# Optimization experiments

Measured on AMD Instinct MI355X. Metric: run time of the kernel, lower is better.

The kernel has to match this reference:

```python
import jax, jax.numpy as jnp
from jax import lax
from jax.experimental.ode import odeint
import numpy as np

INPUT_DIM, HIDDEN_DIM, LATENT_DIM, OUTPUT_DIM = 6, 64, 16, 1
RTOL, ATOL = 1e-3, 1e-4
NOISE_STD = 0.0  # model_noise=0 -> deterministic drift, faithful to relu(W z + b) + 0
B, T = 2048, 512


def _init(key, shape, fan_in):
    bound = 1.0 / np.sqrt(fan_in)
    return jax.random.uniform(key, shape, jnp.float32, -bound, bound)


def setup_inputs() -> dict:
    key = jax.random.key(0)
    ks = jax.random.split(key, 18)
    inp = {
        "x": jax.random.normal(ks[0], (B, T, INPUT_DIM), jnp.float32),
        # encoder GRU (input 6 -> hidden 64), torch layout: W_ih [3H, D], W_hh [3H, H]
        "enc_Wih": _init(ks[1], (3 * HIDDEN_DIM, INPUT_DIM), HIDDEN_DIM),
        "enc_Whh": _init(ks[2], (3 * HIDDEN_DIM, HIDDEN_DIM), HIDDEN_DIM),
        "enc_bih": _init(ks[3], (3 * HIDDEN_DIM,), HIDDEN_DIM),
        "enc_bhh": _init(ks[4], (3 * HIDDEN_DIM,), HIDDEN_DIM),
        "fc_mu_W": _init(ks[5], (LATENT_DIM, HIDDEN_DIM), HIDDEN_DIM),
        "fc_mu_b": _init(ks[6], (LATENT_DIM,), HIDDEN_DIM),
        "fc_lv_W": _init(ks[7], (LATENT_DIM, HIDDEN_DIM), HIDDEN_DIM),
        "fc_lv_b": _init(ks[8], (LATENT_DIM,), HIDDEN_DIM),
        # latent SDE drift linear 16 -> 16
        "ode_W": _init(ks[9], (LATENT_DIM, LATENT_DIM), LATENT_DIM),
        "ode_b": _init(ks[10], (LATENT_DIM,), LATENT_DIM),
        # decoder fc 16 -> 64, then GRU (input 64 -> hidden 1)
        "dec_fc_W": _init(ks[11], (HIDDEN_DIM, LATENT_DIM), LATENT_DIM),
        "dec_fc_b": _init(ks[12], (HIDDEN_DIM,), LATENT_DIM),
        "dec_Wih": _init(ks[13], (3 * OUTPUT_DIM, HIDDEN_DIM), OUTPUT_DIM),
        "dec_Whh": _init(ks[14], (3 * OUTPUT_DIM, OUTPUT_DIM), OUTPUT_DIM),
        "dec_bih": _init(ks[15], (3 * OUTPUT_DIM,), OUTPUT_DIM),
        "dec_bhh": _init(ks[16], (3 * OUTPUT_DIM,), OUTPUT_DIM),
    }
    return inp


def _gru_cell(h, x_gates, Whh, bhh):
    # x_gates: precomputed x @ Wih.T + bih, shape [B, 3H]; h: [B, H]
    h_gates = h @ Whh.T + bhh
    xr, xz, xn = jnp.split(x_gates, 3, axis=-1)
    hr, hz, hn = jnp.split(h_gates, 3, axis=-1)
    r = jax.nn.sigmoid(xr + hr)
    zg = jax.nn.sigmoid(xz + hz)
    n = jnp.tanh(xn + r * hn)
    return (1.0 - zg) * n + zg * h


def _forward(x, enc_Wih, enc_Whh, enc_bih, enc_bhh, fc_mu_W, fc_mu_b,
             fc_lv_W, fc_lv_b, ode_W, ode_b, dec_fc_W, dec_fc_b,
             dec_Wih, dec_Whh, dec_bih, dec_bhh):
    Bsz, Tlen, _ = x.shape
    # ---- encoder GRU, keep only last hidden state ----
    xg = jnp.einsum('btd,gd->btg', x, enc_Wih) + enc_bih  # [B,T,3H]
    h0 = jnp.zeros((Bsz, HIDDEN_DIM), x.dtype)
    def enc_step(h, xt):
        return _gru_cell(h, xt, enc_Whh, enc_bhh), None
    hT, _ = lax.scan(enc_step, h0, jnp.swapaxes(xg, 0, 1))
    mu = hT @ fc_mu_W.T + fc_mu_b          # [B,16]
    log_var = hT @ fc_lv_W.T + fc_lv_b     # [B,16]
    # deterministic reparam exactly as source: z = mu + sqrt(exp(log_var))
    z0 = mu + jnp.exp(0.5 * log_var)
    # ---- dopri5 adaptive integration of dz/dt = relu(W z + b) on t in [0,1] ----
    def drift(z, t):
        return jax.nn.relu(z @ ode_W.T + ode_b)
    ts = jnp.linspace(0.0, 1.0, 10)
    zs = odeint(drift, z0, ts, rtol=RTOL, atol=ATOL)
    z = zs[-1]                              # [B,16]
    # ---- decoder: relu(fc1), repeat over time, GRU(64->1) ----
    zd = jax.nn.relu(z @ dec_fc_W.T + dec_fc_b)            # [B,64]
    xg_dec = zd @ dec_Wih.T + dec_bih                       # same every step, [B,3]
    hd0 = jnp.zeros((Bsz, OUTPUT_DIM), x.dtype)
    def dec_step(h, _):
        h = _gru_cell(h, xg_dec, dec_Whh, dec_bhh)
        return h, h
    _, outs = lax.scan(dec_step, hd0, None, length=Tlen)    # [T,B,1]
    x_recon = jnp.swapaxes(outs, 0, 1)                      # [B,T,1]
    return x_recon, mu, log_var


def reference(x, enc_Wih, enc_Whh, enc_bih, enc_bhh, fc_mu_W, fc_mu_b,
              fc_lv_W, fc_lv_b, ode_W, ode_b, dec_fc_W, dec_fc_b,
              dec_Wih, dec_Whh, dec_bih, dec_bhh):
    return _forward(x, enc_Wih, enc_Whh, enc_bih, enc_bhh, fc_mu_W, fc_mu_b,
                    fc_lv_W, fc_lv_b, ode_W, ode_b, dec_fc_W, dec_fc_b,
                    dec_Wih, dec_Whh, dec_bih, dec_bhh)
```

## Files before the change

### kernel.cpp

```cpp
#include <hip/hip_runtime.h>
#include <math.h>

#define B_TOTAL 2048
#define T_LEN   512
#define IN_D    6
#define HID     64
#define LAT     16
#define ROWS    4
#define THREADS 256
#define ASTRIDE 104

typedef __attribute__((ext_vector_type(8))) short bfrag;
typedef __attribute__((ext_vector_type(4))) float ffrag;

#if __has_builtin(__builtin_amdgcn_exp2f)
#define EXP2F(x) __builtin_amdgcn_exp2f(x)
#else
#define EXP2F(x) exp2f(x)
#endif
#if __has_builtin(__builtin_amdgcn_rcpf)
#define RCPF(x) __builtin_amdgcn_rcpf(x)
#else
#define RCPF(x) (1.0f / (x))
#endif
#define MFMA16(A, B, C) __builtin_amdgcn_mfma_f32_16x16x32_bf16((A), (B), (C), 0, 0, 0)

__device__ __forceinline__ float fast_sigmoid(float x){
    return RCPF(1.0f + EXP2F(-1.44269504088896340736f * x));
}
__device__ __forceinline__ float fast_tanh(float x){
    return 1.0f - 2.0f * RCPF(EXP2F(2.88539008177792681472f * x) + 1.0f);
}
__device__ __forceinline__ unsigned short f2bf_rne(float f){
    unsigned u = __float_as_uint(f);
    return (unsigned short)((u + 0x7fffu + ((u >> 16) & 1u)) >> 16);
}

extern "C" __global__ void
__attribute__((amdgpu_flat_work_group_size(THREADS, THREADS), amdgpu_waves_per_eu(2, 2)))
glsde_kernel(const float* __restrict__ x,
             const float* __restrict__ eWih, const float* __restrict__ eWhh,
             const float* __restrict__ ebih, const float* __restrict__ ebhh,
             const float* __restrict__ muW,  const float* __restrict__ mub,
             const float* __restrict__ lvW,  const float* __restrict__ lvb,
             const float* __restrict__ oW,   const float* __restrict__ ob,
             const float* __restrict__ dfW,  const float* __restrict__ dfb,
             const float* __restrict__ dWih, const float* __restrict__ dWhh,
             const float* __restrict__ dbih, const float* __restrict__ dbhh,
             float* __restrict__ out)
{
    __shared__ __align__(16) unsigned short xstage[T_LEN][ROWS][8];
    __shared__ __align__(16) unsigned short Abuf[2][16][ASTRIDE];
    __shared__ float hfp[ROWS][HID];
    __shared__ float zsh[ROWS][LAT];
    __shared__ float zdsh[ROWS][HID];
    __shared__ float xgdsh[ROWS][3];

    const int tid  = threadIdx.x;
    const int wave = tid >> 6;
    const int lane = tid & 63;
    const int nloc = lane & 15;
    const int quad = lane >> 4;
    const int mA   = lane & 15;
    const int j    = wave * 16 + nloc;
    const int b0   = blockIdx.x * ROWS;

    const float S1 = 1.44269504088896340736f;
    const float S2 = 2.0f * S1;

    bfrag Br[3], Bz[3], Bnh[2], Bnx;
    {
        const float* wr  = eWhh + (size_t)(      j) * HID;
        const float* wz  = eWhh + (size_t)( 64 + j) * HID;
        const float* wn  = eWhh + (size_t)(128 + j) * HID;
        #pragma unroll
        for (int kt = 0; kt < 2; ++kt){
            const int o = kt * 32 + quad * 8;
            #pragma unroll
            for (int e = 0; e < 8; ++e){
                Br[kt][e]  = (short)f2bf_rne(wr[o+e] * S1);
                Bz[kt][e]  = (short)f2bf_rne(wz[o+e] * S1);
                Bnh[kt][e] = (short)f2bf_rne(wn[o+e] * S2);
            }
        }
        const float* ir  = eWih + (size_t)(      j) * IN_D;
        const float* iz  = eWih + (size_t)( 64 + j) * IN_D;
        const float* inn = eWih + (size_t)(128 + j) * IN_D;
        #pragma unroll
        for (int e = 0; e < 8; ++e){
            bool v = (quad == 0 && e < IN_D);
            Br[2][e] = v ? (short)f2bf_rne(ir[e]  * S1) : (short)0;
            Bz[2][e] = v ? (short)f2bf_rne(iz[e]  * S1) : (short)0;
            Bnx[e]   = v ? (short)f2bf_rne(inn[e] * S2) : (short)0;
        }
    }
    const float bias_r = (ebih[j]      + ebhh[j])      * S1;
    const float bias_z = (ebih[64 + j] + ebhh[64 + j]) * S1;
    const float bihn2  = ebih[128 + j] * S2;
    const float bhhn2  = ebhh[128 + j] * S2;

    {
        unsigned* ap = (unsigned*)Abuf;
        for (int i = tid; i < (int)(sizeof(Abuf) / 4); i += THREADS) ap[i] = 0u;
    }

    for (int idx = tid; idx < T_LEN * ROWS; idx += THREADS){
        const int tt = idx & (T_LEN - 1);
        const int bb = idx >> 9;
        const float* xr = x + (size_t)(b0 + bb) * T_LEN * IN_D + (size_t)tt * IN_D;
        const float2* p2 = (const float2*)xr;
        float2 v0 = p2[0], v1 = p2[1], v2 = p2[2];
        bfrag f;
        f[0] = (short)f2bf_rne(v0.x); f[1] = (short)f2bf_rne(v0.y);
        f[2] = (short)f2bf_rne(v1.x); f[3] = (short)f2bf_rne(v1.y);
        f[4] = (short)f2bf_rne(v2.x); f[5] = (short)f2bf_rne(v2.y);
        f[6] = 0; f[7] = 0;
        *(bfrag*)&xstage[tt][bb][0] = f;
    }
    __syncthreads();

    float hreg = 0.f;

    const unsigned short* xsp = &xstage[0][mA >> 2][0];

    bfrag Ax = *(const bfrag*)(xsp);

#define GRU_STEP(bufR, bufW, T)                                                   \
    do {                                                                          \
        const unsigned short* ah_ = &bufR[mA][0];                                 \
        bfrag Ah0 = *(const bfrag*)(ah_ + 0  + quad * 8);                         \
        bfrag Ah1 = *(const bfrag*)(ah_ + 32 + quad * 8);                         \
        int tn_ = (T) + 1; if (tn_ >= T_LEN) tn_ = T_LEN - 1;                     \
        bfrag AxN = *(const bfrag*)(xsp + (size_t)tn_ * (ROWS * 8));              \
        ffrag aR  = {bias_r, bias_r, bias_r, bias_r};                             \
        ffrag aZ  = {bias_z, bias_z, bias_z, bias_z};                             \
        ffrag aNX = {bihn2,  bihn2,  bihn2,  bihn2 };                             \
        ffrag aNH = {bhhn2,  bhhn2,  bhhn2,  bhhn2 };                             \
                      \
        aR  = MFMA16(Ax,  Br[2],  aR );                                           \
        aZ  = MFMA16(Ax,  Bz[2],  aZ );                                           \
        aNX = MFMA16(Ax,  Bnx,    aNX);                                           \
        aR  = MFMA16(Ah0, Br[0],  aR );                                           \
        aZ  = MFMA16(Ah0, Bz[0],  aZ );                                           \
        aNH = MFMA16(Ah0, Bnh[0], aNH);                                           \
        aR  = MFMA16(Ah1, Br[1],  aR );                                           \
        aZ  = MFMA16(Ah1, Bz[1],  aZ );                                           \
        aNH = MFMA16(Ah1, Bnh[1], aNH);                                           \
        float rg = RCPF(1.0f + EXP2F(-aR[0]));                                    \
        float zg = RCPF(1.0f + EXP2F(-aZ[0]));                                    \
        float yy = aNX[0] + rg * aNH[0];                                          \
        float ng = 1.0f - 2.0f * RCPF(EXP2F(yy) + 1.0f);                          \
        float hn = (1.0f - zg) * ng + zg * hreg;                                  \
        hreg = hn;                                                                \
        bufW[quad * 4][j] = f2bf_rne(hn);                                         \
        Ax = AxN;                                                                 \
        __syncthreads();                                                          \
    } while (0)

    for (int t = 0; t < T_LEN; t += 2){
        GRU_STEP(Abuf[0], Abuf[1], t);
        GRU_STEP(Abuf[1], Abuf[0], t + 1);
    }
#undef GRU_STEP

    hfp[quad][j] = hreg;
    __syncthreads();

    const int zrow = tid >> 4, zi = tid & 15;
    float z0v = 0.0f;
    if (tid < ROWS * LAT){
        float am = mub[zi], al = lvb[zi];
        const float4* pm = (const float4*)(muW + (size_t)zi * HID);
        const float4* pq = (const float4*)(lvW + (size_t)zi * HID);
        const float4* ph = (const float4*)(&hfp[zrow][0]);
        #pragma unroll
        for (int q = 0; q < 16; ++q){
            float4 wm = pm[q], wl = pq[q], hv = ph[q];
            am += wm.x*hv.x + wm.y*hv.y + wm.z*hv.z + wm.w*hv.w;
            al += wl.x*hv.x + wl.y*hv.y + wl.z*hv.z + wl.w*hv.w;
        }
        const size_t muBase = (size_t)B_TOTAL * T_LEN;
        out[muBase + (size_t)(b0 + zrow) * LAT + zi] = am;
        out[muBase + (size_t)B_TOTAL * LAT + (size_t)(b0 + zrow) * LAT + zi] = al;
        z0v = am + __expf(0.5f * al);
    }

    if (tid < ROWS * LAT){
        float ows[16];
        {
            const float4* pw = (const float4*)(oW + (size_t)zi * LAT);
            #pragma unroll
            for (int q = 0; q < 4; ++q){
                float4 w = pw[q];
                ows[4*q+0] = w.x; ows[4*q+1] = w.y; ows[4*q+2] = w.z; ows[4*q+3] = w.w;
            }
        }
        const float obv = ob[zi];
        float z = z0v;
        const float hstep = 1.0f / 24.0f;
        for (int s = 0; s < 24; ++s){
            float y, k1, k2, k3, k4;
            y = z;
            { float acc = obv;
              #pragma unroll
              for (int jj = 0; jj < 16; ++jj){ float yj = __shfl(y, jj, 16); acc = fmaf(ows[jj], yj, acc); }
              k1 = fmaxf(acc, 0.0f); }
            y = z + 0.5f * hstep * k1;
            { float acc = obv;
              #pragma unroll
              for (int jj = 0; jj < 16; ++jj){ float yj = __shfl(y, jj, 16); acc = fmaf(ows[jj], yj, acc); }
              k2 = fmaxf(acc, 0.0f); }
            y = z + 0.5f * hstep * k2;
            { float acc = obv;
              #pragma unroll
              for (int jj = 0; jj < 16; ++jj){ float yj = __shfl(y, jj, 16); acc = fmaf(ows[jj], yj, acc); }
              k3 = fmaxf(acc, 0.0f); }
            y = z + hstep * k3;
            { float acc = obv;
              #pragma unroll
              for (int jj = 0; jj < 16; ++jj){ float yj = __shfl(y, jj, 16); acc = fmaf(ows[jj], yj, acc); }
              k4 = fmaxf(acc, 0.0f); }
            z += (hstep / 6.0f) * (k1 + 2.0f*k2 + 2.0f*k3 + k4);
        }
        zsh[zrow][zi] = z;
    }
    __syncthreads();

    for (int idx = tid; idx < ROWS * HID; idx += THREADS){
        const int row = idx >> 6, o = idx & 63;
        float acc = dfb[o];
        const float4* pw = (const float4*)(dfW + (size_t)o * LAT);
        const float4* pz = (const float4*)(&zsh[row][0]);
        #pragma unroll
        for (int q = 0; q < 4; ++q){
            float4 w = pw[q], zv = pz[q];
            acc += w.x*zv.x + w.y*zv.y + w.z*zv.z + w.w*zv.w;
        }
        zdsh[row][o] = fmaxf(acc, 0.0f);
    }
    __syncthreads();

    if (tid < ROWS * 3){
        const int row = tid / 3, gg = tid % 3;
        float acc = dbih[gg];
        const float4* pw = (const float4*)(dWih + (size_t)gg * HID);
        const float4* pz = (const float4*)(&zdsh[row][0]);
        #pragma unroll
        for (int q = 0; q < 16; ++q){
            float4 w = pw[q], zv = pz[q];
            acc += w.x*zv.x + w.y*zv.y + w.z*zv.z + w.w*zv.w;
        }
        xgdsh[row][gg] = acc;
    }
    __syncthreads();

    if (tid < ROWS){
        const int row = tid;
        const float xr = xgdsh[row][0], xz = xgdsh[row][1], xn = xgdsh[row][2];
        const float A0 = dWhh[0], A1 = dWhh[1], A2 = dWhh[2];
        const float c0 = dbhh[0], c1 = dbhh[1], c2 = dbhh[2];
        float* orow = out + (size_t)(b0 + row) * T_LEN;
        float h = 0.0f;
        float ob4[4];
        for (int t = 0; t < T_LEN; ++t){
            float rr = fast_sigmoid(xr + A0 * h + c0);
            float zz = fast_sigmoid(xz + A1 * h + c1);
            float nn = fast_tanh(xn + rr * (A2 * h + c2));
            h = (1.0f - zz) * nn + zz * h;
            ob4[t & 3] = h;
            if ((t & 3) == 3) *(float4*)(orow + (t - 3)) = *(float4*)ob4;
        }
    }
}

extern "C" void kernel_launch(void* const* d_in, const int* in_sizes, int n_in,
                              void* d_out, int out_size, void* d_ws, size_t ws_size,
                              hipStream_t stream){
    glsde_kernel<<<B_TOTAL / ROWS, THREADS, 0, stream>>>(
        (const float*)d_in[0],  (const float*)d_in[1],  (const float*)d_in[2],
        (const float*)d_in[3],  (const float*)d_in[4],  (const float*)d_in[5],
        (const float*)d_in[6],  (const float*)d_in[7],  (const float*)d_in[8],
        (const float*)d_in[9],  (const float*)d_in[10], (const float*)d_in[11],
        (const float*)d_in[12], (const float*)d_in[13], (const float*)d_in[14],
        (const float*)d_in[15], (const float*)d_in[16], (float*)d_out);
}
```

Before: 325.7 us.

## Collapse encoder GRU block to a single wave and drop per-step barriers

Shrinks the workgroup from four waves to one, so a single wave now computes all 64 hidden units of the encoder GRU by looping over four column groups of MFMAs. Because the hidden state is exchanged through LDS inside one wave, the per-timestep __syncthreads can be removed. The aim is to cut barrier latency from the serial recurrence and to give the MFMA pipe four independent accumulator chains to interleave. The cost is four times the MFMA and transcendental work per wave on one SIMD, higher register use from holding all weight fragments, and far fewer waves across the GPU, with many SIMDs left idle.

```diff
diff --git a/kernel.cpp b/kernel.cpp
--- a/kernel.cpp
+++ b/kernel.cpp
@@ -7,7 +7,7 @@
 #define HID     64
 #define LAT     16
 #define ROWS    4
-#define THREADS 256
+#define THREADS 64
 #define ASTRIDE 104
 
 typedef __attribute__((ext_vector_type(8))) short bfrag;
@@ -37,7 +37,7 @@
 }
 
 extern "C" __global__ void
-__attribute__((amdgpu_flat_work_group_size(THREADS, THREADS), amdgpu_waves_per_eu(2, 2)))
+__attribute__((amdgpu_flat_work_group_size(THREADS, THREADS), amdgpu_waves_per_eu(1, 1)))
 glsde_kernel(const float* __restrict__ x,
              const float* __restrict__ eWih, const float* __restrict__ eWhh,
              const float* __restrict__ ebih, const float* __restrict__ ebhh,
@@ -57,53 +57,52 @@
     __shared__ float xgdsh[ROWS][3];
 
     const int tid  = threadIdx.x;
-    const int wave = tid >> 6;
-    const int lane = tid & 63;
-    const int nloc = lane & 15;
-    const int quad = lane >> 4;
-    const int mA   = lane & 15;
-    const int j    = wave * 16 + nloc;
+    const int nloc = tid & 15;
+    const int quad = tid >> 4;
+    const int mA   = tid & 15;
     const int b0   = blockIdx.x * ROWS;
 
     const float S1 = 1.44269504088896340736f;
     const float S2 = 2.0f * S1;
 
-    bfrag Br[3], Bz[3], Bnh[2], Bnx;
-    {
-        const float* wr  = eWhh + (size_t)(      j) * HID;
-        const float* wz  = eWhh + (size_t)( 64 + j) * HID;
-        const float* wn  = eWhh + (size_t)(128 + j) * HID;
+    bfrag Br[4][3], Bz[4][3], Bnh[4][2], Bnx[4];
+    float bias_r[4], bias_z[4], bihn2[4], bhhn2[4];
+    #pragma unroll
+    for (int w = 0; w < 4; ++w){
+        const int jw = w * 16 + nloc;
+        const float* wr  = eWhh + (size_t)(      jw) * HID;
+        const float* wz  = eWhh + (size_t)( 64 + jw) * HID;
+        const float* wn  = eWhh + (size_t)(128 + jw) * HID;
         #pragma unroll
         for (int kt = 0; kt < 2; ++kt){
             const int o = kt * 32 + quad * 8;
             #pragma unroll
             for (int e = 0; e < 8; ++e){
-                Br[kt][e]  = (short)f2bf_rne(wr[o+e] * S1);
-                Bz[kt][e]  = (short)f2bf_rne(wz[o+e] * S1);
-                Bnh[kt][e] = (short)f2bf_rne(wn[o+e] * S2);
+                Br[w][kt][e]  = (short)f2bf_rne(wr[o+e] * S1);
+                Bz[w][kt][e]  = (short)f2bf_rne(wz[o+e] * S1);
+                Bnh[w][kt][e] = (short)f2bf_rne(wn[o+e] * S2);
             }
         }
-        const float* ir  = eWih + (size_t)(      j) * IN_D;
-        const float* iz  = eWih + (size_t)( 64 + j) * IN_D;
-        const float* inn = eWih + (size_t)(128 + j) * IN_D;
+        const float* ir  = eWih + (size_t)(      jw) * IN_D;
+        const float* iz  = eWih + (size_t)( 64 + jw) * IN_D;
+        const float* inn = eWih + (size_t)(128 + jw) * IN_D;
         #pragma unroll
         for (int e = 0; e < 8; ++e){
             bool v = (quad == 0 && e < IN_D);
-            Br[2][e] = v ? (short)f2bf_rne(ir[e]  * S1) : (short)0;
-            Bz[2][e] = v ? (short)f2bf_rne(iz[e]  * S1) : (short)0;
-            Bnx[e]   = v ? (short)f2bf_rne(inn[e] * S2) : (short)0;
-        }
-    }
-    const float bias_r = (ebih[j]      + ebhh[j])      * S1;
-    const float bias_z = (ebih[64 + j] + ebhh[64 + j]) * S1;
-    const float bihn2  = ebih[128 + j] * S2;
-    const float bhhn2  = ebhh[128 + j] * S2;
+            Br[w][2][e] = v ? (short)f2bf_rne(ir[e]  * S1) : (short)0;
+            Bz[w][2][e] = v ? (short)f2bf_rne(iz[e]  * S1) : (short)0;
+            Bnx[w][e]   = v ? (short)f2bf_rne(inn[e] * S2) : (short)0;
+        }
+        bias_r[w] = (ebih[jw]      + ebhh[jw])      * S1;
+        bias_z[w] = (ebih[64 + jw] + ebhh[64 + jw]) * S1;
+        bihn2[w]  = ebih[128 + jw] * S2;
+        bhhn2[w]  = ebhh[128 + jw] * S2;
+    }
 
     {
         unsigned* ap = (unsigned*)Abuf;
         for (int i = tid; i < (int)(sizeof(Abuf) / 4); i += THREADS) ap[i] = 0u;
     }
-
     for (int idx = tid; idx < T_LEN * ROWS; idx += THREADS){
         const int tt = idx & (T_LEN - 1);
         const int bb = idx >> 9;
@@ -119,10 +118,8 @@
     }
     __syncthreads();
 
-    float hreg = 0.f;
-
+    float hreg[4] = {0.f, 0.f, 0.f, 0.f};
     const unsigned short* xsp = &xstage[0][mA >> 2][0];
-
     bfrag Ax = *(const bfrag*)(xsp);
 
 #define GRU_STEP(bufR, bufW, T)                                                   \
@@ -132,29 +129,44 @@
         bfrag Ah1 = *(const bfrag*)(ah_ + 32 + quad * 8);                         \
         int tn_ = (T) + 1; if (tn_ >= T_LEN) tn_ = T_LEN - 1;                     \
         bfrag AxN = *(const bfrag*)(xsp + (size_t)tn_ * (ROWS * 8));              \
-        ffrag aR  = {bias_r, bias_r, bias_r, bias_r};                             \
-        ffrag aZ  = {bias_z, bias_z, bias_z, bias_z};                             \
-        ffrag aNX = {bihn2,  bihn2,  bihn2,  bihn2 };                             \
-        ffrag aNH = {bhhn2,  bhhn2,  bhhn2,  bhhn2 };                             \
-                      \
-        aR  = MFMA16(Ax,  Br[2],  aR );                                           \
-        aZ  = MFMA16(Ax,  Bz[2],  aZ );                                           \
-        aNX = MFMA16(Ax,  Bnx,    aNX);                                           \
-        aR  = MFMA16(Ah0, Br[0],  aR );                                           \
-        aZ  = MFMA16(Ah0, Bz[0],  aZ );                                           \
-        aNH = MFMA16(Ah0, Bnh[0], aNH);                                           \
-        aR  = MFMA16(Ah1, Br[1],  aR );                                           \
-        aZ  = MFMA16(Ah1, Bz[1],  aZ );                                           \
-        aNH = MFMA16(Ah1, Bnh[1], aNH);                                           \
-        float rg = RCPF(1.0f + EXP2F(-aR[0]));                                    \
-        float zg = RCPF(1.0f + EXP2F(-aZ[0]));                                    \
-        float yy = aNX[0] + rg * aNH[0];                                          \
-        float ng = 1.0f - 2.0f * RCPF(EXP2F(yy) + 1.0f);                          \
-        float hn = (1.0f - zg) * ng + zg * hreg;                                  \
-        hreg = hn;                                                                \
-        bufW[quad * 4][j] = f2bf_rne(hn);                                         \
+        ffrag aR[4], aZ[4], aNX[4], aNH[4];                                       \
+        _Pragma("unroll")                                                         \
+        for (int w = 0; w < 4; ++w){                                              \
+            aR[w]  = (ffrag){bias_r[w], bias_r[w], bias_r[w], bias_r[w]};         \
+            aZ[w]  = (ffrag){bias_z[w], bias_z[w], bias_z[w], bias_z[w]};         \
+            aNX[w] = (ffrag){bihn2[w],  bihn2[w],  bihn2[w],  bihn2[w] };         \
+            aNH[w] = (ffrag){bhhn2[w],  bhhn2[w],  bhhn2[w],  bhhn2[w] };         \
+        }                                                                         \
+              \
+        _Pragma("unroll")                                                         \
+        for (int w = 0; w < 4; ++w){                                              \
+            aR[w]  = MFMA16(Ax, Br[w][2], aR[w]);                                 \
+            aZ[w]  = MFMA16(Ax, Bz[w][2], aZ[w]);                                 \
+            aNX[w] = MFMA16(Ax, Bnx[w],   aNX[w]);                                \
+        }                                                                         \
+        _Pragma("unroll")                                                         \
+        for (int w = 0; w < 4; ++w){                                              \
+            aR[w]  = MFMA16(Ah0, Br[w][0],  aR[w]);                               \
+            aZ[w]  = MFMA16(Ah0, Bz[w][0],  aZ[w]);                               \
+            aNH[w] = MFMA16(Ah0, Bnh[w][0], aNH[w]);                              \
+        }                                                                         \
+        _Pragma("unroll")                                                         \
+        for (int w = 0; w < 4; ++w){                                              \
+            aR[w]  = MFMA16(Ah1, Br[w][1],  aR[w]);                               \
+            aZ[w]  = MFMA16(Ah1, Bz[w][1],  aZ[w]);                               \
+            aNH[w] = MFMA16(Ah1, Bnh[w][1], aNH[w]);                              \
+        }                                                                         \
+        _Pragma("unroll")                                                         \
+        for (int w = 0; w < 4; ++w){                                              \
+            float rg = RCPF(1.0f + EXP2F(-aR[w][0]));                             \
+            float zg = RCPF(1.0f + EXP2F(-aZ[w][0]));                             \
+            float yy = aNX[w][0] + rg * aNH[w][0];                                \
+            float ng = 1.0f - 2.0f * RCPF(EXP2F(yy) + 1.0f);                      \
+            float hn = (1.0f - zg) * ng + zg * hreg[w];                           \
+            hreg[w] = hn;                                                         \
+            bufW[quad * 4][w * 16 + nloc] = f2bf_rne(hn);                         \
+        }                                                                         \
         Ax = AxN;                                                                 \
-        __syncthreads();                                                          \
     } while (0)
 
     for (int t = 0; t < T_LEN; t += 2){
@@ -163,12 +175,13 @@
     }
 #undef GRU_STEP
 
-    hfp[quad][j] = hreg;
+    #pragma unroll
+    for (int w = 0; w < 4; ++w) hfp[quad][w * 16 + nloc] = hreg[w];
     __syncthreads();
 
     const int zrow = tid >> 4, zi = tid & 15;
     float z0v = 0.0f;
-    if (tid < ROWS * LAT){
+    {
         float am = mub[zi], al = lvb[zi];
         const float4* pm = (const float4*)(muW + (size_t)zi * HID);
         const float4* pq = (const float4*)(lvW + (size_t)zi * HID);
@@ -185,7 +198,7 @@
         z0v = am + __expf(0.5f * al);
     }
 
-    if (tid < ROWS * LAT){
+    {
         float ows[16];
         {
             const float4* pw = (const float4*)(oW + (size_t)zi * LAT);
```

After: 441.0 us. 35.4% more time.
